# Kernel optimization log

Hardware: AMD Instinct MI355X
Metric: run time of the kernel (lower is better)

The kernel has to match this reference:

```python
import jax, jax.numpy as jnp
import numpy as np

B = 2048
D = 40960          # util.half_kp_numel(): 64 king squares * 640 piece-square planes
BASE = 288
MOVE = 4096        # util.move_numel(): 64 from-squares * 64 to-squares
MOVE_SIZE = (64, 64)


def setup_inputs() -> dict:
    key = jax.random.key(0)
    ks = jax.random.split(key, 24)
    f32 = jnp.float32
    # forward args: sparse one-hot half-kp occupancy vectors (modeled as rand floats)
    pov = (jax.random.uniform(ks[0], (B, 1), f32) > 0.5).astype(f32)
    white = (jax.random.uniform(ks[1], (B, D), f32) < 0.001).astype(f32)
    black = (jax.random.uniform(ks[2], (B, D), f32) < 0.001).astype(f32)
    s = 0.01
    p = {
        'W_w': jax.random.normal(ks[3], (BASE, D), f32) * s,
        'b_w': jnp.zeros((BASE,), f32),
        'W_b': jax.random.normal(ks[4], (BASE, D), f32) * s,
        'b_b': jnp.zeros((BASE,), f32),
        'W_v0': jax.random.normal(ks[5], (32, 2 * BASE), f32) * s,
        'b_v0': jnp.zeros((32,), f32),
        'W_v1': jax.random.normal(ks[6], (32, 32), f32) * s,
        'b_v1': jnp.zeros((32,), f32),
        'W_v2': jax.random.normal(ks[7], (1, 32), f32) * s,
        'b_v2': jnp.zeros((1,), f32),
        'W_a0': jax.random.normal(ks[8], (144, 2 * BASE), f32) * s,
        'b_a0': jnp.zeros((144,), f32),
        'W_a1': jax.random.normal(ks[9], (MOVE, 144), f32) * s,
        'b_a1': jnp.zeros((MOVE,), f32),
        'W_vs': jax.random.normal(ks[10], (1, 2 * BASE), f32) * s,
        'b_vs': jnp.zeros((1,), f32),
        'W_as': jax.random.normal(ks[11], (MOVE, 2 * BASE), f32) * s,
        'b_as': jnp.zeros((MOVE,), f32),
    }
    return dict(pov=pov, white=white, black=black, **p)


def _linear(x, W, b):
    return x @ W.T + b


def reference(pov, white, black, W_w, b_w, W_b, b_b,
              W_v0, b_v0, W_v1, b_v1, W_v2, b_v2,
              W_a0, b_a0, W_a1, b_a1, W_vs, b_vs, W_as, b_as):
    # half-kp affine accumulators (the sparse gather-sum candidate)
    w256 = _linear(white, W_w, b_w)            # [B, BASE]
    b256 = _linear(black, W_b, b_b)            # [B, BASE]
    cat_wb = jnp.concatenate([w256, b256], axis=1)
    cat_bw = jnp.concatenate([b256, w256], axis=1)
    base = jax.nn.relu(pov * cat_wb + (1.0 - pov) * cat_bw)  # [B, 2*BASE]
    # value head with skip
    val = jax.nn.relu(_linear(base, W_v0, b_v0))
    val = jax.nn.relu(_linear(val, W_v1, b_v1))
    val = _linear(val, W_v2, b_v2) + _linear(base, W_vs, b_vs)   # [B, 1]
    # action head with skip
    act = jax.nn.relu(_linear(base, W_a0, b_a0))
    act = _linear(act, W_a1, b_a1) + _linear(base, W_as, b_as)   # [B, MOVE]
    act = act.reshape(act.shape[0], *MOVE_SIZE)                  # [B, 64, 64]
    return (val, act)
```

## Files before the change

### kernel.cpp

```cpp
#include <hip/hip_runtime.h>

#define D_IN 40960
#define NB 2048
#define BASEN 288
#define CAPL 95
#define KP 736

typedef __attribute__((ext_vector_type(4))) float f32x4;
typedef __attribute__((ext_vector_type(8))) short short8;

__device__ inline float bf2f(ushort u) {
    unsigned v = ((unsigned)u) << 16; float f; __builtin_memcpy(&f, &v, 4); return f;
}
__device__ inline ushort f2bf(float f) {
    unsigned x; __builtin_memcpy(&x, &f, 4);
    unsigned r = (x + 0x7FFFu + ((x >> 16) & 1u)) >> 16; return (ushort)r;
}

__device__ inline void llds16(const void* g, void* l) {
    __builtin_amdgcn_global_load_lds((const __attribute__((address_space(1))) unsigned*)g,
                                     (__attribute__((address_space(3))) unsigned*)l, 16, 0, 0);
}

__global__ __launch_bounds__(256) void transpose_kernel(const float* __restrict__ Ww,
                                                        const float* __restrict__ Wb,
                                                        ushort* __restrict__ Wtw,
                                                        ushort* __restrict__ Wtb) {
    const float* src = blockIdx.z ? Wb : Ww;
    ushort* dst = blockIdx.z ? Wtb : Wtw;
    __shared__ float tile[32][65];
    int i = threadIdx.x;
    int d0 = blockIdx.x * 64, o0 = blockIdx.y * 32;
    int tr = i >> 4, tc4 = (i & 15) * 4;
#pragma unroll
    for (int rep = 0; rep < 2; ++rep) {
        int row = tr + rep * 16;
        float4 u = *(const float4*)&src[(size_t)(o0 + row) * D_IN + d0 + tc4];
        tile[row][tc4] = u.x; tile[row][tc4 + 1] = u.y; tile[row][tc4 + 2] = u.z; tile[row][tc4 + 3] = u.w;
    }
    __syncthreads();
    int dr = i >> 3, oc4 = (i & 7) * 4;
#pragma unroll
    for (int rep = 0; rep < 2; ++rep) {
        int d = dr + rep * 32;
        ushort4 u;
        u.x = f2bf(tile[oc4][d]); u.y = f2bf(tile[oc4 + 1][d]);
        u.z = f2bf(tile[oc4 + 2][d]); u.w = f2bf(tile[oc4 + 3][d]);
        *(ushort4*)&dst[(size_t)(d0 + d) * BASEN + o0 + oc4] = u;
    }
}

__global__ __launch_bounds__(256) void prep_kernel(const float* __restrict__ W_a1,
                                                   const float* __restrict__ W_as,
                                                   const float* __restrict__ b_a1,
                                                   const float* __restrict__ b_as,
                                                   const float* __restrict__ W_a0,
                                                   const float* __restrict__ W_v0,
                                                   ushort* __restrict__ Wcat,
                                                   float* __restrict__ biasA,
                                                   ushort* __restrict__ Wa0h,
                                                   ushort* __restrict__ Wv0h) {
    int m = blockIdx.x, t = threadIdx.x;
    if (m < 4096) {
        ushort* dst = Wcat + (size_t)m * KP;
        if (t < 144) dst[t] = f2bf(W_a1[(size_t)m * 144 + t]);
        if (t >= 144 && t < 160) dst[t] = 0;
        for (int j = t; j < 576; j += 256) dst[160 + j] = f2bf(W_as[(size_t)m * 576 + j]);
        if (t == 200) biasA[m] = b_a1[m] + b_as[m];
    } else if (m < 4096 + 144) {
        int r = m - 4096;
        for (int j = t; j < 576; j += 256) Wa0h[(size_t)r * 576 + j] = f2bf(W_a0[(size_t)r * 576 + j]);
    } else {
        int r = m - (4096 + 144);
        for (int j = t; j < 576; j += 256) Wv0h[(size_t)r * 576 + j] = f2bf(W_v0[(size_t)r * 576 + j]);
    }
}

__global__ __launch_bounds__(576) void row_kernel(const float* __restrict__ white,
                                                  const float* __restrict__ black,
                                                  const ushort* __restrict__ Wtw,
                                                  const ushort* __restrict__ Wtb,
                                                  const float* __restrict__ pov,
                                                  const float* __restrict__ b_w,
                                                  const float* __restrict__ b_b,
                                                  const ushort* __restrict__ Wa0h,
                                                  const float* __restrict__ b_a0,
                                                  const ushort* __restrict__ Wv0h,
                                                  const float* __restrict__ b_v0,
                                                  const float* __restrict__ W_v1,
                                                  const float* __restrict__ b_v1,
                                                  const float* __restrict__ W_v2,
                                                  const float* __restrict__ b_v2,
                                                  const float* __restrict__ W_vs,
                                                  const float* __restrict__ b_vs,
                                                  ushort* __restrict__ hidden,
                                                  float* __restrict__ outv) {
    int b = blockIdx.x, t = threadIdx.x;
    __shared__ int cntW, cntB;
    __shared__ int idxW[CAPL], idxB[CAPL];
    __shared__ float accS[576];
    __shared__ float baseS[576];
    __shared__ float v0s[32];
    __shared__ float skipS;
    if (t == 0) cntW = 0;
    if (t == 1) cntB = 0;
    __syncthreads();

    {
        const uint4* vw = (const uint4*)(white + (size_t)b * D_IN);
        const uint4* vb = (const uint4*)(black + (size_t)b * D_IN);
        const int NV = D_IN / 4;
#pragma unroll
        for (int base = 0; base < NV; base += 576 * 4) {
            uint4 xw[4], xb[4];
            int id[4];
#pragma unroll
            for (int u = 0; u < 4; ++u) {
                int i = base + u * 576 + t;
                id[u] = i;
                int ic = i < NV ? i : NV - 1;
                xw[u] = vw[ic];
                xb[u] = vb[ic];
            }
#pragma unroll
            for (int u = 0; u < 4; ++u) {
                bool valid = id[u] < NV;
                uint4 x = xw[u];
                if (valid && (x.x | x.y | x.z | x.w)) {
                    int i4 = id[u] * 4;
                    if (x.x) { int p = atomicAdd(&cntW, 1); if (p < CAPL) idxW[p] = i4; }
                    if (x.y) { int p = atomicAdd(&cntW, 1); if (p < CAPL) idxW[p] = i4 + 1; }
                    if (x.z) { int p = atomicAdd(&cntW, 1); if (p < CAPL) idxW[p] = i4 + 2; }
                    if (x.w) { int p = atomicAdd(&cntW, 1); if (p < CAPL) idxW[p] = i4 + 3; }
                }
                uint4 y = xb[u];
                if (valid && (y.x | y.y | y.z | y.w)) {
                    int i4 = id[u] * 4;
                    if (y.x) { int p = atomicAdd(&cntB, 1); if (p < CAPL) idxB[p] = i4; }
                    if (y.y) { int p = atomicAdd(&cntB, 1); if (p < CAPL) idxB[p] = i4 + 1; }
                    if (y.z) { int p = atomicAdd(&cntB, 1); if (p < CAPL) idxB[p] = i4 + 2; }
                    if (y.w) { int p = atomicAdd(&cntB, 1); if (p < CAPL) idxB[p] = i4 + 3; }
                }
            }
        }
    }
    __syncthreads();

    {
        int col = (t < 288) ? t : t - 288;
        const ushort* Wt = (t < 288) ? Wtw : Wtb;
        const int* il = (t < 288) ? idxW : idxB;
        int n = min((t < 288) ? cntW : cntB, CAPL);
        float acc = (t < 288) ? b_w[col] : b_b[col];
#pragma unroll 4
        for (int i = 0; i < n; ++i) acc += bf2f(Wt[(size_t)il[i] * BASEN + col]);
        accS[t] = acc;
    }
    __syncthreads();

    float p = pov[b];
    ushort* hrow = hidden + (size_t)b * KP;
    if (t < 288) {
        float aW = accS[t], aB = accS[288 + t];
        float b0 = fmaxf(p * aW + (1.0f - p) * aB, 0.0f);
        float b1 = fmaxf(p * aB + (1.0f - p) * aW, 0.0f);
        baseS[t] = b0; baseS[288 + t] = b1;
        hrow[160 + t] = f2bf(b0);
        hrow[160 + 288 + t] = f2bf(b1);
        if (t < 16) hrow[144 + t] = 0;
    }
    __syncthreads();

    {
        int o = t >> 2, q4 = t & 3;
        const ushort* wr = Wa0h + (size_t)o * 576 + q4 * 144;
        const float* bp = &baseS[q4 * 144];
        float s = 0.f;
#pragma unroll
        for (int j = 0; j < 144; j += 8) {
            uint4 q = *(const uint4*)(wr + j);
            s += bp[j + 0] * bf2f((ushort)(q.x & 0xFFFF)) + bp[j + 1] * bf2f((ushort)(q.x >> 16))
               + bp[j + 2] * bf2f((ushort)(q.y & 0xFFFF)) + bp[j + 3] * bf2f((ushort)(q.y >> 16))
               + bp[j + 4] * bf2f((ushort)(q.z & 0xFFFF)) + bp[j + 5] * bf2f((ushort)(q.z >> 16))
               + bp[j + 6] * bf2f((ushort)(q.w & 0xFFFF)) + bp[j + 7] * bf2f((ushort)(q.w >> 16));
        }
        s += __shfl_xor(s, 1);
        s += __shfl_xor(s, 2);
        if (q4 == 0) hrow[o] = f2bf(fmaxf(s + b_a0[o], 0.f));
    }

    if (t < 512) {
        int o = t >> 4, sub = t & 15;
        const ushort* wr = Wv0h + (size_t)o * 576 + sub * 36;
        const float* bp = &baseS[sub * 36];
        float s = 0.f;
#pragma unroll
        for (int j = 0; j < 36; j += 4) {
            ushort4 q = *(const ushort4*)(wr + j);
            s += bp[j + 0] * bf2f(q.x) + bp[j + 1] * bf2f(q.y)
               + bp[j + 2] * bf2f(q.z) + bp[j + 3] * bf2f(q.w);
        }
        s += __shfl_xor(s, 1); s += __shfl_xor(s, 2);
        s += __shfl_xor(s, 4); s += __shfl_xor(s, 8);
        if (sub == 0) v0s[o] = fmaxf(s + b_v0[o], 0.f);
    } else {
        int u = t - 512;
        const float* wp = W_vs + u * 9;
        const float* bp = &baseS[u * 9];
        float s = 0.f;
#pragma unroll
        for (int j = 0; j < 9; ++j) s += bp[j] * wp[j];
        s += __shfl_xor(s, 1); s += __shfl_xor(s, 2); s += __shfl_xor(s, 4);
        s += __shfl_xor(s, 8); s += __shfl_xor(s, 16); s += __shfl_xor(s, 32);
        if (u == 0) skipS = s;
    }
    __syncthreads();

    if (t < 32) {
        float s = b_v1[t];
        const float* w = W_v1 + (size_t)t * 32;
#pragma unroll
        for (int j = 0; j < 32; ++j) s += v0s[j] * w[j];
        float part = fmaxf(s, 0.f) * W_v2[t];
        part += __shfl_xor(part, 1); part += __shfl_xor(part, 2); part += __shfl_xor(part, 4);
        part += __shfl_xor(part, 8); part += __shfl_xor(part, 16);
        if (t == 0) outv[b] = part + b_v2[0] + skipS + b_vs[0];
    }
}

__global__ __launch_bounds__(256) void gemm_act(const ushort* __restrict__ A,
                                                const ushort* __restrict__ Bm,
                                                const float* __restrict__ biasA,
                                                float* __restrict__ outa) {
    __shared__ ushort As[128 * 32];
    __shared__ ushort Bs[128 * 32];
    int tid = threadIdx.x;
    int lane = tid & 63, wv = tid >> 6;
    int bm = blockIdx.x, bn = blockIdx.y;
    int wm = wv & 1, wn = wv >> 1;
    f32x4 acc[4][4];
#pragma unroll
    for (int mt = 0; mt < 4; ++mt)
#pragma unroll
        for (int nt = 0; nt < 4; ++nt) { f32x4 z = {0.f, 0.f, 0.f, 0.f}; acc[mt][nt] = z; }

    int r = tid >> 2, c8 = (tid & 3) * 8;
    const ushort* Ag = A  + (size_t)(bm * 128 + r) * KP + c8;
    const ushort* Bg = Bm + (size_t)(bn * 128 + r) * KP + c8;
    ushort* AsW = As + wv * 512;
    ushort* BsW = Bs + wv * 512;

    int kg = (lane >> 4) * 8;
    int rA = wm * 64 + (lane & 15);
    int rB = wn * 64 + (lane & 15);

    for (int kk = 0; kk < KP; kk += 32) {
        llds16(Ag + kk, AsW);
        llds16(Ag + (size_t)64 * KP + kk, AsW + 2048);
        llds16(Bg + kk, BsW);
        llds16(Bg + (size_t)64 * KP + kk, BsW + 2048);
        __syncthreads();
        short8 af[4], bf[4];
#pragma unroll
        for (int mt = 0; mt < 4; ++mt) af[mt] = *(const short8*)&As[(rA + mt * 16) * 32 + kg];
#pragma unroll
        for (int nt = 0; nt < 4; ++nt) bf[nt] = *(const short8*)&Bs[(rB + nt * 16) * 32 + kg];
#pragma unroll
        for (int mt = 0; mt < 4; ++mt)
#pragma unroll
            for (int nt = 0; nt < 4; ++nt)
                acc[mt][nt] = __builtin_amdgcn_mfma_f32_16x16x32_bf16(af[mt], bf[nt], acc[mt][nt], 0, 0, 0);
        __syncthreads();
    }

    int colb = bn * 128 + wn * 64 + (lane & 15);
    int rowb = bm * 128 + wm * 64 + ((lane >> 4) << 2);
#pragma unroll
    for (int nt = 0; nt < 4; ++nt) {
        float bia = biasA[colb + nt * 16];
#pragma unroll
        for (int mt = 0; mt < 4; ++mt) {
#pragma unroll
            for (int q = 0; q < 4; ++q) {
                int rr = rowb + mt * 16 + q;
                outa[(size_t)rr * 4096 + colb + nt * 16] = acc[mt][nt][q] + bia;
            }
        }
    }
}

extern "C" void kernel_launch(void* const* d_in, const int* in_sizes, int n_in,
                              void* d_out, int out_size, void* d_ws, size_t ws_size,
                              hipStream_t stream) {
    const float* pov   = (const float*)d_in[0];
    const float* white = (const float*)d_in[1];
    const float* black = (const float*)d_in[2];
    const float* W_w   = (const float*)d_in[3];
    const float* b_w   = (const float*)d_in[4];
    const float* W_b   = (const float*)d_in[5];
    const float* b_b   = (const float*)d_in[6];
    const float* W_v0  = (const float*)d_in[7];
    const float* b_v0  = (const float*)d_in[8];
    const float* W_v1  = (const float*)d_in[9];
    const float* b_v1  = (const float*)d_in[10];
    const float* W_v2  = (const float*)d_in[11];
    const float* b_v2  = (const float*)d_in[12];
    const float* W_a0  = (const float*)d_in[13];
    const float* b_a0  = (const float*)d_in[14];
    const float* W_a1  = (const float*)d_in[15];
    const float* b_a1  = (const float*)d_in[16];
    const float* W_vs  = (const float*)d_in[17];
    const float* b_vs  = (const float*)d_in[18];
    const float* W_as  = (const float*)d_in[19];
    const float* b_as  = (const float*)d_in[20];

    char* ws = (char*)d_ws;
    ushort* Wtw   = (ushort*)(ws + 0);
    ushort* Wtb   = (ushort*)(ws + 23592960);
    ushort* hidden= (ushort*)(ws + 47185920);
    ushort* Wcat  = (ushort*)(ws + 50200576);
    float*  biasA = (float*)(ws + 56229888);
    ushort* Wa0h  = (ushort*)(ws + 56246272);
    ushort* Wv0h  = (ushort*)(ws + 56412160);

    float* outp = (float*)d_out;

    transpose_kernel<<<dim3(D_IN / 64, BASEN / 32, 2), 256, 0, stream>>>(W_w, W_b, Wtw, Wtb);
    prep_kernel<<<4096 + 144 + 32, 256, 0, stream>>>(W_a1, W_as, b_a1, b_as, W_a0, W_v0,
                                                     Wcat, biasA, Wa0h, Wv0h);
    row_kernel<<<NB, 576, 0, stream>>>(white, black, Wtw, Wtb, pov, b_w, b_b,
                                       Wa0h, b_a0, Wv0h, b_v0, W_v1, b_v1, W_v2, b_v2,
                                       W_vs, b_vs, hidden, outp);
    gemm_act<<<dim3(2048 / 128, 4096 / 128), 256, 0, stream>>>(hidden, Wcat, biasA, outp + 2048);
}
```

Baseline: 829.2 us.

## Split row kernel into per-side scan kernel and separate head kernel

The fused per-row kernel is split in two. The first scans the white and black occupancy rows in separate 320-thread blocks on a 2D grid and writes the gathered accumulators to a global buffer. The second reads those accumulators and runs the value and action heads. This doubles the number of blocks streaming the large dense input and gives the scan deeper per-thread loads, in exchange for an extra kernel launch and a global round trip of the accumulators.

```diff
diff --git a/kernel.cpp b/kernel.cpp
--- a/kernel.cpp
+++ b/kernel.cpp
@@ -76,97 +76,81 @@
     }
 }
 
-__global__ __launch_bounds__(576) void row_kernel(const float* __restrict__ white,
-                                                  const float* __restrict__ black,
-                                                  const ushort* __restrict__ Wtw,
-                                                  const ushort* __restrict__ Wtb,
-                                                  const float* __restrict__ pov,
-                                                  const float* __restrict__ b_w,
-                                                  const float* __restrict__ b_b,
-                                                  const ushort* __restrict__ Wa0h,
-                                                  const float* __restrict__ b_a0,
-                                                  const ushort* __restrict__ Wv0h,
-                                                  const float* __restrict__ b_v0,
-                                                  const float* __restrict__ W_v1,
-                                                  const float* __restrict__ b_v1,
-                                                  const float* __restrict__ W_v2,
-                                                  const float* __restrict__ b_v2,
-                                                  const float* __restrict__ W_vs,
-                                                  const float* __restrict__ b_vs,
-                                                  ushort* __restrict__ hidden,
-                                                  float* __restrict__ outv) {
+__global__ __launch_bounds__(320) void scan_kernel(const float* __restrict__ white,
+                                                   const float* __restrict__ black,
+                                                   const ushort* __restrict__ Wtw,
+                                                   const ushort* __restrict__ Wtb,
+                                                   const float* __restrict__ b_w,
+                                                   const float* __restrict__ b_b,
+                                                   float* __restrict__ accG) {
+    const int row = blockIdx.x;
+    const int colr = blockIdx.y;
+    const int t = threadIdx.x;
+    __shared__ int cnt;
+    __shared__ int idx[CAPL];
+    if (t == 0) cnt = 0;
+    __syncthreads();
+
+    const uint4* src = (const uint4*)((colr ? black : white) + (size_t)row * D_IN);
+    const int NV = D_IN / 4;
+#pragma unroll
+    for (int base = 0; base < NV; base += 320 * 8) {
+        uint4 x[8];
+#pragma unroll
+        for (int u = 0; u < 8; ++u) x[u] = src[base + u * 320 + t];
+#pragma unroll
+        for (int u = 0; u < 8; ++u) {
+            uint4 v = x[u];
+            if (v.x | v.y | v.z | v.w) {
+                int i4 = (base + u * 320 + t) * 4;
+                if (v.x) { int p = atomicAdd(&cnt, 1); if (p < CAPL) idx[p] = i4; }
+                if (v.y) { int p = atomicAdd(&cnt, 1); if (p < CAPL) idx[p] = i4 + 1; }
+                if (v.z) { int p = atomicAdd(&cnt, 1); if (p < CAPL) idx[p] = i4 + 2; }
+                if (v.w) { int p = atomicAdd(&cnt, 1); if (p < CAPL) idx[p] = i4 + 3; }
+            }
+        }
+    }
+    __syncthreads();
+
+    if (t < BASEN) {
+        const ushort* Wt = colr ? Wtb : Wtw;
+        int n = min(cnt, CAPL);
+        float acc = colr ? b_b[t] : b_w[t];
+#pragma unroll 4
+        for (int i = 0; i < n; ++i) acc += bf2f(Wt[(size_t)idx[i] * BASEN + t]);
+        accG[((size_t)colr * NB + row) * BASEN + t] = acc;
+    }
+}
+
+__global__ __launch_bounds__(576) void head_kernel(const float* __restrict__ accG,
+                                                   const float* __restrict__ pov,
+                                                   const ushort* __restrict__ Wa0h,
+                                                   const float* __restrict__ b_a0,
+                                                   const ushort* __restrict__ Wv0h,
+                                                   const float* __restrict__ b_v0,
+                                                   const float* __restrict__ W_v1,
+                                                   const float* __restrict__ b_v1,
+                                                   const float* __restrict__ W_v2,
+                                                   const float* __restrict__ b_v2,
+                                                   const float* __restrict__ W_vs,
+                                                   const float* __restrict__ b_vs,
+                                                   ushort* __restrict__ hidden,
+                                                   float* __restrict__ outv) {
     int b = blockIdx.x, t = threadIdx.x;
-    __shared__ int cntW, cntB;
-    __shared__ int idxW[CAPL], idxB[CAPL];
-    __shared__ float accS[576];
     __shared__ float baseS[576];
     __shared__ float v0s[32];
     __shared__ float skipS;
-    if (t == 0) cntW = 0;
-    if (t == 1) cntB = 0;
-    __syncthreads();
-
-    {
-        const uint4* vw = (const uint4*)(white + (size_t)b * D_IN);
-        const uint4* vb = (const uint4*)(black + (size_t)b * D_IN);
-        const int NV = D_IN / 4;
-#pragma unroll
-        for (int base = 0; base < NV; base += 576 * 4) {
-            uint4 xw[4], xb[4];
-            int id[4];
-#pragma unroll
-            for (int u = 0; u < 4; ++u) {
-                int i = base + u * 576 + t;
-                id[u] = i;
-                int ic = i < NV ? i : NV - 1;
-                xw[u] = vw[ic];
-                xb[u] = vb[ic];
-            }
-#pragma unroll
-            for (int u = 0; u < 4; ++u) {
-                bool valid = id[u] < NV;
-                uint4 x = xw[u];
-                if (valid && (x.x | x.y | x.z | x.w)) {
-                    int i4 = id[u] * 4;
-                    if (x.x) { int p = atomicAdd(&cntW, 1); if (p < CAPL) idxW[p] = i4; }
-                    if (x.y) { int p = atomicAdd(&cntW, 1); if (p < CAPL) idxW[p] = i4 + 1; }
-                    if (x.z) { int p = atomicAdd(&cntW, 1); if (p < CAPL) idxW[p] = i4 + 2; }
-                    if (x.w) { int p = atomicAdd(&cntW, 1); if (p < CAPL) idxW[p] = i4 + 3; }
-                }
-                uint4 y = xb[u];
-                if (valid && (y.x | y.y | y.z | y.w)) {
-                    int i4 = id[u] * 4;
-                    if (y.x) { int p = atomicAdd(&cntB, 1); if (p < CAPL) idxB[p] = i4; }
-                    if (y.y) { int p = atomicAdd(&cntB, 1); if (p < CAPL) idxB[p] = i4 + 1; }
-                    if (y.z) { int p = atomicAdd(&cntB, 1); if (p < CAPL) idxB[p] = i4 + 2; }
-                    if (y.w) { int p = atomicAdd(&cntB, 1); if (p < CAPL) idxB[p] = i4 + 3; }
-                }
-            }
-        }
-    }
-    __syncthreads();
-
-    {
-        int col = (t < 288) ? t : t - 288;
-        const ushort* Wt = (t < 288) ? Wtw : Wtb;
-        const int* il = (t < 288) ? idxW : idxB;
-        int n = min((t < 288) ? cntW : cntB, CAPL);
-        float acc = (t < 288) ? b_w[col] : b_b[col];
-#pragma unroll 4
-        for (int i = 0; i < n; ++i) acc += bf2f(Wt[(size_t)il[i] * BASEN + col]);
-        accS[t] = acc;
-    }
-    __syncthreads();
 
     float p = pov[b];
     ushort* hrow = hidden + (size_t)b * KP;
-    if (t < 288) {
-        float aW = accS[t], aB = accS[288 + t];
+    if (t < BASEN) {
+        float aW = accG[(size_t)b * BASEN + t];
+        float aB = accG[(size_t)NB * BASEN + (size_t)b * BASEN + t];
         float b0 = fmaxf(p * aW + (1.0f - p) * aB, 0.0f);
         float b1 = fmaxf(p * aB + (1.0f - p) * aW, 0.0f);
-        baseS[t] = b0; baseS[288 + t] = b1;
+        baseS[t] = b0; baseS[BASEN + t] = b1;
         hrow[160 + t] = f2bf(b0);
-        hrow[160 + 288 + t] = f2bf(b1);
+        hrow[160 + BASEN + t] = f2bf(b1);
         if (t < 16) hrow[144 + t] = 0;
     }
     __syncthreads();
@@ -322,14 +306,15 @@
     float*  biasA = (float*)(ws + 56229888);
     ushort* Wa0h  = (ushort*)(ws + 56246272);
     ushort* Wv0h  = (ushort*)(ws + 56412160);
+    float*  accG  = (float*)(ws + 56449024);
 
     float* outp = (float*)d_out;
 
     transpose_kernel<<<dim3(D_IN / 64, BASEN / 32, 2), 256, 0, stream>>>(W_w, W_b, Wtw, Wtb);
     prep_kernel<<<4096 + 144 + 32, 256, 0, stream>>>(W_a1, W_as, b_a1, b_as, W_a0, W_v0,
                                                      Wcat, biasA, Wa0h, Wv0h);
-    row_kernel<<<NB, 576, 0, stream>>>(white, black, Wtw, Wtb, pov, b_w, b_b,
-                                       Wa0h, b_a0, Wv0h, b_v0, W_v1, b_v1, W_v2, b_v2,
-                                       W_vs, b_vs, hidden, outp);
+    scan_kernel<<<dim3(NB, 2), 320, 0, stream>>>(white, black, Wtw, Wtb, b_w, b_b, accG);
+    head_kernel<<<NB, 576, 0, stream>>>(accG, pov, Wa0h, b_a0, Wv0h, b_v0,
+                                        W_v1, b_v1, W_v2, b_v2, W_vs, b_vs, hidden, outp);
     gemm_act<<<dim3(2048 / 128, 4096 / 128), 256, 0, stream>>>(hidden, Wcat, biasA, outp + 2048);
 }
```

After: 846.0 us. 2.0% more time.
